# Optimization experiments

Hardware: AMD Instinct MI355X
Metric: run time of the kernel (lower is better)

The kernel has to match this reference:

```python
import jax, jax.numpy as jnp
import numpy as np

VOCAB_SIZE = 14        # digits 0-9, '.', '-', ' ', '<pad>'
D_MODEL = 128
T = 131072             # number of timesteps (strings)
TOTAL_CHARS = 1572864  # ~12 chars per serialized value, flattened


def setup_inputs() -> dict:
    key = jax.random.key(0)
    k1, k2, k3 = jax.random.split(key, 3)
    # xavier_uniform init for the char embedding table, as in the torch module
    limit = np.sqrt(6.0 / (VOCAB_SIZE + D_MODEL)).astype(np.float32)
    char_emb = jax.random.uniform(k1, (VOCAB_SIZE, D_MODEL), jnp.float32, -limit, limit)
    # flat character index stream (each value in [0, 14))
    char_indices = jax.random.randint(k2, (TOTAL_CHARS,), 0, VOCAB_SIZE, dtype=jnp.int64)
    # sorted segment ids: which timestep each character belongs to (ragged lengths)
    segment_ids = jnp.sort(jax.random.randint(k3, (TOTAL_CHARS,), 0, T, dtype=jnp.int64))
    return {"char_emb": char_emb, "char_indices": char_indices,
            "segment_ids": segment_ids, "T": T}


def reference(char_emb, char_indices, segment_ids, T):
    # 1) embedding gather for every character: [N, d_model]
    chars = char_emb[char_indices]
    # 2) fused segment mean over ragged strings -> [T, d_model]
    sums = jax.ops.segment_sum(chars, segment_ids, num_segments=T)
    counts = jax.ops.segment_sum(jnp.ones((char_indices.shape[0],), chars.dtype),
                                 segment_ids, num_segments=T)
    # torch strings always have >=1 char; guard empty segments from random ids
    return sums / jnp.maximum(counts, 1.0)[:, None]
```

## Files before the change

### kernel.cpp

```cpp
#include <hip/hip_runtime.h>
#include <hip/hip_bf16.h>


#define D_MODEL 128
#define VOCAB 14
#define CPB 1024
#define NSLOT 272
#define HSTRIDE 16

__global__ __launch_bounds__(256, 4) void fused_seg_mean_kernel(
        const float* __restrict__ emb,
        const int* __restrict__ idx,
        const int* __restrict__ seg,
        float* __restrict__ out, int N, int T) {
    __shared__ int h[NSLOT * HSTRIDE];

    const int tid  = threadIdx.x;
    const int c0   = blockIdx.x * CPB;
    const int lane = tid & 63;
    const int wave = tid >> 6;
    const int sub  = lane & 31;
    const int half = lane >> 5;

    const int  prev          = (c0 == 0) ? -1 : seg[c0 - 1];
    const int  last          = min(c0 + CPB - 1, N - 1);
    const int  t_hi          = seg[last];
    const bool is_last_block = (last == N - 1);
    const int  t_hi_own      = is_last_block ? (T - 1) : t_hi;
    const int  own           = t_hi_own - prev;
    if (own <= 0) return;

    float4 e4[VOCAB];
    #pragma unroll
    for (int v = 0; v < VOCAB; ++v)
        e4[v] = *(const float4*)&emb[v * D_MODEL + 4 * sub];

    const int span_stream = t_hi - prev;

    if (span_stream <= NSLOT) {
        for (int i = tid; i < NSLOT * HSTRIDE; i += 256) h[i] = 0;
        __syncthreads();

        int base = c0 + tid * 4;
        int s4[4], i4[4];
        if (base + 3 < N) {
            int4 sv = *(const int4*)(seg + base);
            int4 iv = *(const int4*)(idx + base);
            s4[0] = sv.x; s4[1] = sv.y; s4[2] = sv.z; s4[3] = sv.w;
            i4[0] = iv.x; i4[1] = iv.y; i4[2] = iv.z; i4[3] = iv.w;
        } else {
            for (int k = 0; k < 4; ++k) {
                s4[k] = (base + k < N) ? seg[base + k] : -1;
                i4[k] = (base + k < N) ? idx[base + k] : 0;
            }
        }
        #pragma unroll
        for (int k = 0; k < 4; ++k) {
            int s = s4[k];
            if (s > prev)
                atomicAdd(&h[((s - prev - 1) << 4) + i4[k]], 1);
        }
        if (wave == 0 && !is_last_block) {
            int p = c0 + CPB;
            while (p < N) {
                int pp = p + lane;
                int ss = (pp < N) ? seg[pp] : 0x7fffffff;
                if (ss == t_hi)
                    atomicAdd(&h[((t_hi - prev - 1) << 4) + idx[pp]], 1);
                if (__shfl(ss, 63) != t_hi) break;
                p += 64;
            }
        }
        __syncthreads();

        for (int p = wave * 2; p < own; p += 8) {
            int tloc = p + half;
            float4 acc = make_float4(0.f, 0.f, 0.f, 0.f);
            float total = 0.f;
            if (tloc < span_stream) {
                const int* hp = &h[tloc << 4];
                int4 a = *(const int4*)(hp + 0);
                int4 b = *(const int4*)(hp + 4);
                int4 c = *(const int4*)(hp + 8);
                int4 d = *(const int4*)(hp + 12);
                int cn[VOCAB] = {a.x, a.y, a.z, a.w, b.x, b.y, b.z, b.w,
                                 c.x, c.y, c.z, c.w, d.x, d.y};
                #pragma unroll
                for (int v = 0; v < VOCAB; ++v) {
                    float f = (float)cn[v];
                    total += f;
                    acc.x += f * e4[v].x;
                    acc.y += f * e4[v].y;
                    acc.z += f * e4[v].z;
                    acc.w += f * e4[v].w;
                }
            }
            if (tloc < own) {
                float inv = 1.0f / fmaxf(total, 1.0f);
                int t = prev + 1 + tloc;
                *(float4*)&out[(size_t)t * D_MODEL + 4 * sub] =
                    make_float4(acc.x * inv, acc.y * inv, acc.z * inv, acc.w * inv);
            }
        }
    } else {
        for (int p = wave * 2; p < own; p += 8) {
            int tloc = p + half;
            bool active = tloc < own;
            int t = prev + 1 + tloc;
            int cn[VOCAB];
            #pragma unroll
            for (int v = 0; v < VOCAB; ++v) cn[v] = 0;
            int q = c0;
            while (q < N) {
                int qq = q + sub;
                int ss = (qq < N) ? seg[qq] : 0x7fffffff;
                int ii = (qq < N) ? idx[qq] : 0xff;
                #pragma unroll
                for (int v = 0; v < VOCAB; ++v) {
                    unsigned long long m = __ballot(active && ss == t && ii == v);
                    cn[v] += __popcll(half ? (m >> 32) : (m & 0xffffffffull));
                }
                if (__shfl(ss, 31) > prev + 2 + p) break;
                q += 32;
            }
            float4 acc = make_float4(0.f, 0.f, 0.f, 0.f);
            float total = 0.f;
            #pragma unroll
            for (int v = 0; v < VOCAB; ++v) {
                float f = (float)cn[v];
                total += f;
                acc.x += f * e4[v].x;
                acc.y += f * e4[v].y;
                acc.z += f * e4[v].z;
                acc.w += f * e4[v].w;
            }
            if (active) {
                float inv = 1.0f / fmaxf(total, 1.0f);
                *(float4*)&out[(size_t)t * D_MODEL + 4 * sub] =
                    make_float4(acc.x * inv, acc.y * inv, acc.z * inv, acc.w * inv);
            }
        }
    }
}

extern "C" void kernel_launch(void* const* d_in, const int* in_sizes, int n_in,
                              void* d_out, int out_size, void* d_ws, size_t ws_size,
                              hipStream_t stream) {
    const float* char_emb     = (const float*)d_in[0];
    const int*   char_indices = (const int*)d_in[1];
    const int*   segment_ids  = (const int*)d_in[2];
    float*       out          = (float*)d_out;

    int N = in_sizes[1];
    int T = out_size / D_MODEL;

    int nblk = (N + CPB - 1) / CPB;
    fused_seg_mean_kernel<<<nblk, 256, 0, stream>>>(
        char_emb, char_indices, segment_ids, out, N, T);
}
```

Before: 95.05 us.

## Split fused kernel into histogram and emit kernels with packed byte counts

Splits the single fused kernel into two launches. The first builds per-block character histograms in shared memory and writes them to workspace packed as 8-bit counts per vocab entry, plus a small per-block header. The second reads those packed counts and writes the output, with no shared memory, so more blocks can be resident and the heavy histogram and output-write phases no longer compete for shared memory. This adds a second launch, a global round trip for the histograms and header, and assumes each segment/vocab count fits in 8 bits.

```diff
diff --git a/kernel.cpp b/kernel.cpp
--- a/kernel.cpp
+++ b/kernel.cpp
@@ -7,20 +7,21 @@
 #define CPB 1024
 #define NSLOT 272
 #define HSTRIDE 16
+#define HDW (NSLOT * 4)
 
-__global__ __launch_bounds__(256, 4) void fused_seg_mean_kernel(
-        const float* __restrict__ emb,
+__global__ __launch_bounds__(256) void hist_kernel(
         const int* __restrict__ idx,
         const int* __restrict__ seg,
-        float* __restrict__ out, int N, int T) {
+        int4* __restrict__ hdr,
+        unsigned int* __restrict__ hist,
+        int N, int T) {
     __shared__ int h[NSLOT * HSTRIDE];
 
     const int tid  = threadIdx.x;
-    const int c0   = blockIdx.x * CPB;
+    const int b    = blockIdx.x;
+    const int c0   = b * CPB;
     const int lane = tid & 63;
     const int wave = tid >> 6;
-    const int sub  = lane & 31;
-    const int half = lane >> 5;
 
     const int  prev          = (c0 == 0) ? -1 : seg[c0 - 1];
     const int  last          = min(c0 + CPB - 1, N - 1);
@@ -28,6 +29,74 @@
     const bool is_last_block = (last == N - 1);
     const int  t_hi_own      = is_last_block ? (T - 1) : t_hi;
     const int  own           = t_hi_own - prev;
+    const int  span          = t_hi - prev;
+
+    if (tid == 0) hdr[b] = make_int4(prev, own, span, 0);
+    if (own <= 0 || span > NSLOT) return;
+
+    for (int i = tid; i < span * HSTRIDE; i += 256) h[i] = 0;
+    __syncthreads();
+
+    int base = c0 + tid * 4;
+    int s4[4], i4[4];
+    if (base + 3 < N) {
+        int4 sv = *(const int4*)(seg + base);
+        int4 iv = *(const int4*)(idx + base);
+        s4[0] = sv.x; s4[1] = sv.y; s4[2] = sv.z; s4[3] = sv.w;
+        i4[0] = iv.x; i4[1] = iv.y; i4[2] = iv.z; i4[3] = iv.w;
+    } else {
+        for (int k = 0; k < 4; ++k) {
+            s4[k] = (base + k < N) ? seg[base + k] : -1;
+            i4[k] = (base + k < N) ? idx[base + k] : 0;
+        }
+    }
+    #pragma unroll
+    for (int k = 0; k < 4; ++k) {
+        int s = s4[k];
+        if (s > prev)
+            atomicAdd(&h[((s - prev - 1) << 4) + i4[k]], 1);
+    }
+    if (wave == 0 && !is_last_block) {
+        int p = c0 + CPB;
+        while (p < N) {
+            int pp = p + lane;
+            int ss = (pp < N) ? seg[pp] : 0x7fffffff;
+            if (ss == t_hi)
+                atomicAdd(&h[((t_hi - prev - 1) << 4) + idx[pp]], 1);
+            if (__shfl(ss, 63) != t_hi) break;
+            p += 64;
+        }
+    }
+    __syncthreads();
+
+    unsigned int* hb = hist + (size_t)b * HDW;
+    for (int s = tid; s < span; s += 256) {
+        const int* hp = &h[s << 4];
+        uint4 w;
+        w.x = (unsigned)hp[0]  | ((unsigned)hp[1]  << 8) | ((unsigned)hp[2]  << 16) | ((unsigned)hp[3]  << 24);
+        w.y = (unsigned)hp[4]  | ((unsigned)hp[5]  << 8) | ((unsigned)hp[6]  << 16) | ((unsigned)hp[7]  << 24);
+        w.z = (unsigned)hp[8]  | ((unsigned)hp[9]  << 8) | ((unsigned)hp[10] << 16) | ((unsigned)hp[11] << 24);
+        w.w = (unsigned)hp[12] | ((unsigned)hp[13] << 8);
+        *(uint4*)&hb[s * 4] = w;
+    }
+}
+
+__global__ __launch_bounds__(256, 4) void emit_kernel(
+        const float* __restrict__ emb,
+        const int* __restrict__ idx,
+        const int* __restrict__ seg,
+        const int4* __restrict__ hdr,
+        const unsigned int* __restrict__ hist,
+        float* __restrict__ out, int N, int T) {
+    const int tid  = threadIdx.x;
+    const int b    = blockIdx.x;
+    const int lane = tid & 63;
+    const int wave = tid >> 6;
+    const int sub  = lane & 31;
+    const int half = lane >> 5;
+
+    const int4 H    = hdr[b];
+    const int  prev = H.x, own = H.y, span = H.z;
     if (own <= 0) return;
 
     float4 e4[VOCAB];
@@ -35,59 +104,18 @@
     for (int v = 0; v < VOCAB; ++v)
         e4[v] = *(const float4*)&emb[v * D_MODEL + 4 * sub];
 
-    const int span_stream = t_hi - prev;
-
-    if (span_stream <= NSLOT) {
-        for (int i = tid; i < NSLOT * HSTRIDE; i += 256) h[i] = 0;
-        __syncthreads();
-
-        int base = c0 + tid * 4;
-        int s4[4], i4[4];
-        if (base + 3 < N) {
-            int4 sv = *(const int4*)(seg + base);
-            int4 iv = *(const int4*)(idx + base);
-            s4[0] = sv.x; s4[1] = sv.y; s4[2] = sv.z; s4[3] = sv.w;
-            i4[0] = iv.x; i4[1] = iv.y; i4[2] = iv.z; i4[3] = iv.w;
-        } else {
-            for (int k = 0; k < 4; ++k) {
-                s4[k] = (base + k < N) ? seg[base + k] : -1;
-                i4[k] = (base + k < N) ? idx[base + k] : 0;
-            }
-        }
-        #pragma unroll
-        for (int k = 0; k < 4; ++k) {
-            int s = s4[k];
-            if (s > prev)
-                atomicAdd(&h[((s - prev - 1) << 4) + i4[k]], 1);
-        }
-        if (wave == 0 && !is_last_block) {
-            int p = c0 + CPB;
-            while (p < N) {
-                int pp = p + lane;
-                int ss = (pp < N) ? seg[pp] : 0x7fffffff;
-                if (ss == t_hi)
-                    atomicAdd(&h[((t_hi - prev - 1) << 4) + idx[pp]], 1);
-                if (__shfl(ss, 63) != t_hi) break;
-                p += 64;
-            }
-        }
-        __syncthreads();
-
+    if (span <= NSLOT) {
+        const unsigned int* hb = hist + (size_t)b * HDW;
         for (int p = wave * 2; p < own; p += 8) {
             int tloc = p + half;
             float4 acc = make_float4(0.f, 0.f, 0.f, 0.f);
             float total = 0.f;
-            if (tloc < span_stream) {
-                const int* hp = &h[tloc << 4];
-                int4 a = *(const int4*)(hp + 0);
-                int4 b = *(const int4*)(hp + 4);
-                int4 c = *(const int4*)(hp + 8);
-                int4 d = *(const int4*)(hp + 12);
-                int cn[VOCAB] = {a.x, a.y, a.z, a.w, b.x, b.y, b.z, b.w,
-                                 c.x, c.y, c.z, c.w, d.x, d.y};
+            if (tloc < span) {
+                uint4 w = *(const uint4*)&hb[tloc * 4];
+                unsigned cw[4] = {w.x, w.y, w.z, w.w};
                 #pragma unroll
                 for (int v = 0; v < VOCAB; ++v) {
-                    float f = (float)cn[v];
+                    float f = (float)((cw[v >> 2] >> ((v & 3) * 8)) & 0xffu);
                     total += f;
                     acc.x += f * e4[v].x;
                     acc.y += f * e4[v].y;
@@ -103,6 +131,7 @@
             }
         }
     } else {
+        const int c0 = b * CPB;
         for (int p = wave * 2; p < own; p += 8) {
             int tloc = p + half;
             bool active = tloc < own;
@@ -118,7 +147,7 @@
                 #pragma unroll
                 for (int v = 0; v < VOCAB; ++v) {
                     unsigned long long m = __ballot(active && ss == t && ii == v);
-                    cn[v] += __popcll(half ? (m >> 32) : (m & 0xffffffffull));
+                    cn[v] += __popcll(half ? (unsigned)(m >> 32) : (unsigned)(m & 0xffffffffull));
                 }
                 if (__shfl(ss, 31) > prev + 2 + p) break;
                 q += 32;
@@ -153,8 +182,13 @@
 
     int N = in_sizes[1];
     int T = out_size / D_MODEL;
+    int nblk = (N + CPB - 1) / CPB;
 
-    int nblk = (N + CPB - 1) / CPB;
-    fused_seg_mean_kernel<<<nblk, 256, 0, stream>>>(
-        char_emb, char_indices, segment_ids, out, N, T);
+    int4*         hdr  = (int4*)d_ws;
+    unsigned int* hist = (unsigned int*)((char*)d_ws + (size_t)nblk * sizeof(int4));
+
+    hist_kernel<<<nblk, 256, 0, stream>>>(
+        char_indices, segment_ids, hdr, hist, N, T);
+    emit_kernel<<<nblk, 256, 0, stream>>>(
+        char_emb, char_indices, segment_ids, hdr, hist, out, N, T);
 }
```

After: 100.0 us. 5.2% more time.
